# Performance work log

Hardware: AMD Instinct MI355X
Metric: run time of the kernel (lower is better)

The kernel has to match this reference:

```python
import jax, jax.numpy as jnp
import numpy as np

B = 1024            # batch of CIFAR images (== number of routed tokens, seq_len is 1)
D = 768             # d_model (switch-base-8)
FF = 3072           # d_ff
E = 8               # num experts
L = 12              # encoder layers; odd-indexed layers are sparse MoE (sparse_step=2)
NM = L // 2         # 6 MoE layers and 6 dense FFN layers
NUM_CLASSES = 10


def setup_inputs() -> dict:
    key = jax.random.key(0)
    ks = jax.random.split(key, 12)
    s = 0.02
    return {
        "x": jax.random.normal(ks[0], (B, 3, 32, 32), jnp.float32),
        "proj_w": jax.random.normal(ks[1], (3 * 32 * 32, D), jnp.float32) * s,
        "proj_b": jnp.zeros((D,), jnp.float32),
        "ln1_w": jnp.ones((L, D), jnp.float32),
        "wv": jax.random.normal(ks[2], (L, D, D), jnp.float32) * s,
        "wo": jax.random.normal(ks[3], (L, D, D), jnp.float32) * s,
        "ln2_w": jnp.ones((L, D), jnp.float32),
        "dwi": jax.random.normal(ks[4], (NM, D, FF), jnp.float32) * s,
        "dwo": jax.random.normal(ks[5], (NM, FF, D), jnp.float32) * s,
        "router_w": jax.random.normal(ks[6], (NM, D, E), jnp.float32) * s,
        "ewi": jax.random.normal(ks[7], (NM, E, D, FF), jnp.float32) * s,
        "ewo": jax.random.normal(ks[8], (NM, E, FF, D), jnp.float32) * s,
        "final_ln_w": jnp.ones((D,), jnp.float32),
        "fc_w": jax.random.normal(ks[9], (D, NUM_CLASSES), jnp.float32) * s,
        "fc_b": jnp.zeros((NUM_CLASSES,), jnp.float32),
    }


def rms_norm(h, w, eps=1e-6):
    # T5LayerNorm: RMS norm, no mean subtraction, no bias
    var = jnp.mean(jnp.square(h), axis=-1, keepdims=True)
    return w * (h * jax.lax.rsqrt(var + eps))


def reference(x, proj_w, proj_b, ln1_w, wv, wo, ln2_w, dwi, dwo,
              router_w, ewi, ewo, final_ln_w, fc_w, fc_b):
    # flatten image, project to d_model; unsqueeze(1) in torch -> one token per image,
    # so we keep tokens as [B, D] throughout.
    h = x.reshape(x.shape[0], -1) @ proj_w + proj_b              # [B, D]
    d_i = 0
    m_i = 0
    for layer in range(L):
        # --- self-attention block. seq_len == 1 => softmax over a single key is
        #     identically 1 (for any scores / position bias), so the attention
        #     output is exactly Wo(Wv(x_norm)); q/k projections drop out of the
        #     math (and carry zero gradient).
        n = rms_norm(h, ln1_w[layer])
        h = h + (n @ wv[layer]) @ wo[layer]
        # --- feed-forward block (pre-norm, residual) ---
        n = rms_norm(h, ln2_w[layer])
        if layer % 2 == 1:
            # Switch top-1 MoE. With seq_len==1, token_priority==1 <= expert
            # capacity, so no tokens are ever dropped; every token goes to its
            # argmax expert and is scaled by the router probability.
            logits = n @ router_w[m_i]                           # [B, E]
            probs = jax.nn.softmax(logits, axis=-1)
            top_prob = jnp.max(probs, axis=-1, keepdims=True)    # [B, 1]
            disp = jax.nn.one_hot(jnp.argmax(probs, axis=-1), E, dtype=n.dtype)  # [B, E]
            # dense reference for the sparse dispatch: run every expert, then
            # combine with the one-hot routing mask (same math as gather/scatter)
            hid = jax.nn.relu(jnp.einsum('bd,edf->ebf', n, ewi[m_i]))   # [E, B, FF]
            eout = jnp.einsum('ebf,efd->ebd', hid, ewo[m_i])            # [E, B, D]
            moe = jnp.einsum('ebd,be->bd', eout, disp)                  # [B, D]
            h = h + top_prob * moe
            m_i += 1
        else:
            h = h + jax.nn.relu(n @ dwi[d_i]) @ dwo[d_i]
            d_i += 1
    h = rms_norm(h, final_ln_w)
    return h @ fc_w + fc_b                                      # [B, 10] logits
```

## Files before the change

kernel.cpp:

```cpp
#include <hip/hip_runtime.h>
#include <type_traits>

#define DEV __device__ __forceinline__

typedef _Float16 f16;
typedef __attribute__((ext_vector_type(8))) _Float16 f16x8;
typedef __attribute__((ext_vector_type(4))) float f32x4;

constexpr int NP = 48;

DEV int imin(int a, int b) { return a < b ? a : b; }

DEV int swz(int row, int colByte) { return (row * 128 + colByte) ^ ((row & 7) << 4); }

DEV void split2(float x, float y, unsigned& hi, unsigned& lo) {
  f16 hx = (f16)x, hy = (f16)y;
  f16 lx = (f16)(x - (float)hx), ly = (f16)(y - (float)hy);
  hi = (unsigned)__builtin_bit_cast(unsigned short, hx) |
       ((unsigned)__builtin_bit_cast(unsigned short, hy) << 16);
  lo = (unsigned)__builtin_bit_cast(unsigned short, lx) |
       ((unsigned)__builtin_bit_cast(unsigned short, ly) << 16);
}

DEV void lgkm_barrier() {
  asm volatile("s_waitcnt lgkmcnt(0)" ::: "memory");
  __builtin_amdgcn_s_barrier();
  asm volatile("" ::: "memory");
}

struct GArgs {
  const void* A; const void* Alo;
  const void* B; const void* Blo;
  const float* Hin; float* Hout;
  f16* O16; f16* O16lo;
  const float* rspIn; float* rspOut;
  const float* lnw;
  const float* prob; const float* bias;
  const int* perm; const int* off;
  int M, K, lda, ldb, ldo;
  long sAz, sBz, sOz;
  long zA, zB, zH;
  int KS;
};

template<int TM,int TN,int WR,int WC,int AM,int BMD,int CM,bool RESID,bool BIAS,bool EXPERT>
DEV void gk_body(GArgs a) {
  constexpr int TK = 64;
  constexpr int NT = 256;
  static_assert(WR * WC == 4, "4 waves per block");
  constexpr int WTM = TM / WR, WTN = TN / WC;
  constexpr int FM = WTM / 16, FN = WTN / 16;
  constexpr bool APAIR = (AM == 0);
  constexpr int UA = APAIR ? (TM * (TK / 8)) / NT : (TM * (TK / 4)) / NT;
  constexpr int UB = (TN * (TK / 4)) / NT;

  __shared__ __align__(16) f16 As[2 * TM * TK];
  __shared__ __align__(16) f16 Bs[2 * TN * TK];
  __shared__ __align__(16) f16 AsL[2 * TM * TK];
  __shared__ __align__(16) f16 BsL[2 * TN * TK];
  __shared__ float rrlds[(AM == 2 || AM == 3) ? TM : 1];

  const int tid = threadIdx.x;
  const int lane = tid & 63;
  const int wid = tid >> 6;
  const int wr = wid / WC, wc = wid % WC;

  int m0;
  int sEnd = 0x7fffffff;
  const char* Ab = (const char*)a.A;
  const char* AbL = (const char*)a.Alo;
  const char* Bb = (const char*)a.B;
  f16* O = a.O16;
  f16* OL = a.O16lo;
  float* HoutP = a.Hout;
  {
    int z = blockIdx.z;
    int e = z / a.KS;
    int kc = z - e * a.KS;
    if constexpr (EXPERT) {
      int o0 = a.off[e], o1 = a.off[e + 1];
      if ((int)blockIdx.y * TM >= o1 - o0) return;
      m0 = o0 + blockIdx.y * TM;
      sEnd = o1;
      Bb += (long)e * a.sBz * 4 + (long)kc * a.zB;
      Ab += (long)kc * a.zA;
      AbL += (long)kc * a.zA;
    } else {
      m0 = blockIdx.y * TM;
      Ab += (long)e * a.sAz * 4 + (long)kc * a.zA;
      AbL += (long)kc * a.zA;
      Bb += (long)e * a.sBz * 4 + (long)kc * a.zB;
    }
    if constexpr (CM == 4) HoutP += (long)kc * a.zH;
  }
  const int n0 = blockIdx.x * TN;

  if constexpr (AM == 2 || AM == 3) {
    if (tid < TM) {
      int s = m0 + tid;
      int row = (AM == 3) ? a.perm[imin(s, a.M - 1)] : imin(s, a.M - 1);
      float ss = 0.f;
      #pragma unroll
      for (int j = 0; j < NP; ++j) ss += a.rspIn[row * NP + j];
      rrlds[tid] = rsqrtf(ss * (1.f / 768.f) + 1e-6f);
    }
  }

  int arow[UA];
  #pragma unroll
  for (int u = 0; u < UA; ++u) {
    int id = tid + u * NT;
    if constexpr (AM == 0) arow[u] = imin(m0 + (id >> 3), a.M - 1);
    else if constexpr (AM == 3) arow[u] = a.perm[imin(m0 + (id >> 4), a.M - 1)];
    else arow[u] = imin(m0 + (id >> 4), a.M - 1);
  }

  using ARt = typename std::conditional<APAIR, int4, float4>::type;
  using BRt = float4;

  auto issueA = [&](ARt* rg, ARt* rl, int k0) {
    #pragma unroll
    for (int u = 0; u < UA; ++u) {
      int id = tid + u * NT;
      if constexpr (APAIR) {
        int kq = id & 7;
        long off = ((long)arow[u] * a.lda + k0 + kq * 8) * 2;
        rg[u] = *(const int4*)(Ab + off);
        rl[u] = *(const int4*)(AbL + off);
      } else {
        int kq = id & 15;
        rg[u] = *(const float4*)(Ab + ((long)arow[u] * a.lda + k0 + kq * 4) * 4);
      }
    }
  };
  auto commitA = [&](ARt* rg, ARt* rl, int k0, int bi) {
    char* base = (char*)As + bi * (TM * 128);
    char* baseL = (char*)AsL + bi * (TM * 128);
    #pragma unroll
    for (int u = 0; u < UA; ++u) {
      int id = tid + u * NT;
      if constexpr (APAIR) {
        int m = id >> 3, kq = id & 7;
        *(int4*)(base + swz(m, kq * 16)) = rg[u];
        *(int4*)(baseL + swz(m, kq * 16)) = rl[u];
      } else {
        int m = id >> 4, kq = id & 15;
        float4 v = *(float4*)&rg[u];
        if constexpr (AM == 2 || AM == 3) {
          float rr = rrlds[m];
          const float* w = a.lnw + k0 + kq * 4;
          v.x *= rr * w[0]; v.y *= rr * w[1]; v.z *= rr * w[2]; v.w *= rr * w[3];
        }
        uint2 ph, pl;
        split2(v.x, v.y, ph.x, pl.x);
        split2(v.z, v.w, ph.y, pl.y);
        *(uint2*)(base + swz(m, kq * 8)) = ph;
        *(uint2*)(baseL + swz(m, kq * 8)) = pl;
      }
    }
  };
  auto issueB = [&](BRt* rg, int k0) {
    #pragma unroll
    for (int u = 0; u < UB; ++u) {
      int id = tid + u * NT;
      int n = id % TN, kq = id / TN;
      const float* g = (const float*)Bb;
      #pragma unroll
      for (int i = 0; i < 4; ++i)
        ((float*)&rg[u])[i] = g[(long)(k0 + kq * 4 + i) * a.ldb + (n0 + n)];
    }
  };
  auto commitB = [&](BRt* rg, int bi) {
    char* base = (char*)Bs + bi * (TN * 128);
    char* baseL = (char*)BsL + bi * (TN * 128);
    #pragma unroll
    for (int u = 0; u < UB; ++u) {
      int id = tid + u * NT;
      int n = id % TN, kq = id / TN;
      float4 v = *(float4*)&rg[u];
      uint2 ph, pl;
      split2(v.x, v.y, ph.x, pl.x);
      split2(v.z, v.w, ph.y, pl.y);
      *(uint2*)(base + swz(n, kq * 8)) = ph;
      *(uint2*)(baseL + swz(n, kq * 8)) = pl;
    }
  };

  f32x4 acc[FM][FN] = {};
  auto compute = [&](int bi) {
    const char* pA = (const char*)As + bi * (TM * 128);
    const char* pAL = (const char*)AsL + bi * (TM * 128);
    const char* pB = (const char*)Bs + bi * (TN * 128);
    const char* pBL = (const char*)BsL + bi * (TN * 128);
    #pragma unroll
    for (int kk = 0; kk < 2; ++kk) {
      const int col2 = (kk * 32 + (lane >> 4) * 8) * 2;
      f16x8 ah[FM], al[FM], bh[FN], bl[FN];
      #pragma unroll
      for (int i = 0; i < FM; ++i) {
        ah[i] = *(const f16x8*)(pA + swz(wr * WTM + i * 16 + (lane & 15), col2));
        al[i] = *(const f16x8*)(pAL + swz(wr * WTM + i * 16 + (lane & 15), col2));
      }
      #pragma unroll
      for (int j = 0; j < FN; ++j) {
        bh[j] = *(const f16x8*)(pB + swz(wc * WTN + j * 16 + (lane & 15), col2));
        bl[j] = *(const f16x8*)(pBL + swz(wc * WTN + j * 16 + (lane & 15), col2));
      }
      #pragma unroll
      for (int i = 0; i < FM; ++i)
        #pragma unroll
        for (int j = 0; j < FN; ++j) {
          f32x4 t = acc[i][j];
          t = __builtin_amdgcn_mfma_f32_16x16x32_f16(al[i], bh[j], t, 0, 0, 0);
          t = __builtin_amdgcn_mfma_f32_16x16x32_f16(ah[i], bl[j], t, 0, 0, 0);
          t = __builtin_amdgcn_mfma_f32_16x16x32_f16(ah[i], bh[j], t, 0, 0, 0);
          acc[i][j] = t;
        }
    }
  };

  ARt ag0[UA], ag1[UA], ag2[UA], al0[UA], al1[UA], al2[UA];
  BRt bg0[UB], bg1[UB], bg2[UB];
  const int ns = a.K / TK;
  issueA(ag0, al0, 0); issueB(bg0, 0);
  if (TK < a.K) { issueA(ag1, al1, TK); issueB(bg1, TK); }
  __syncthreads();
  for (int s = 0; s < ns; s += 6) {
    int k;
    { commitA(ag0, al0, (s + 0) * TK, 0); commitB(bg0, 0);
      k = (s + 2) * TK; if (k < a.K) { issueA(ag2, al2, k); issueB(bg2, k); }
      lgkm_barrier(); compute(0); }
    if (s + 1 < ns) {
      commitA(ag1, al1, (s + 1) * TK, 1); commitB(bg1, 1);
      k = (s + 3) * TK; if (k < a.K) { issueA(ag0, al0, k); issueB(bg0, k); }
      lgkm_barrier(); compute(1); }
    if (s + 2 < ns) {
      commitA(ag2, al2, (s + 2) * TK, 0); commitB(bg2, 0);
      k = (s + 4) * TK; if (k < a.K) { issueA(ag1, al1, k); issueB(bg1, k); }
      lgkm_barrier(); compute(0); }
    if (s + 3 < ns) {
      commitA(ag0, al0, (s + 3) * TK, 1); commitB(bg0, 1);
      k = (s + 5) * TK; if (k < a.K) { issueA(ag2, al2, k); issueB(bg2, k); }
      lgkm_barrier(); compute(1); }
    if (s + 4 < ns) {
      commitA(ag1, al1, (s + 4) * TK, 0); commitB(bg1, 0);
      k = (s + 6) * TK; if (k < a.K) { issueA(ag0, al0, k); issueB(bg0, k); }
      lgkm_barrier(); compute(0); }
    if (s + 5 < ns) {
      commitA(ag2, al2, (s + 5) * TK, 1); commitB(bg2, 1);
      k = (s + 7) * TK; if (k < a.K) { issueA(ag1, al1, k); issueB(bg1, k); }
      lgkm_barrier(); compute(1); }
  }

  const int cr = (lane >> 4) * 4;
  const int cc = lane & 15;
  if constexpr (CM == 0 || CM == 2) {
    #pragma unroll
    for (int i = 0; i < FM; ++i) {
      #pragma unroll
      for (int r = 0; r < 4; ++r) {
        int gm = m0 + wr * WTM + i * 16 + cr + r;
        if (gm >= sEnd) continue;
        #pragma unroll
        for (int j = 0; j < FN; ++j) {
          int gn = n0 + wc * WTN + j * 16 + cc;
          float v = acc[i][j][r];
          if constexpr (CM == 2) v = fmaxf(v, 0.f);
          f16 hv = (f16)v;
          O[(long)gm * a.ldo + gn] = hv;
          OL[(long)gm * a.ldo + gn] = (f16)(v - (float)hv);
        }
      }
    }
  } else if constexpr (CM == 4) {
    #pragma unroll
    for (int i = 0; i < FM; ++i) {
      #pragma unroll
      for (int r = 0; r < 4; ++r) {
        int s = m0 + wr * WTM + i * 16 + cr + r;
        if (s >= sEnd || s >= a.M) continue;
        #pragma unroll
        for (int j = 0; j < FN; ++j) {
          int gn = n0 + wc * WTN + j * 16 + cc;
          HoutP[(long)s * a.ldo + gn] = acc[i][j][r];
        }
      }
    }
  } else {
    #pragma unroll
    for (int i = 0; i < FM; ++i) {
      #pragma unroll
      for (int r = 0; r < 4; ++r) {
        int s = m0 + wr * WTM + i * 16 + cr + r;
        int grow = s;
        float p = 1.f;
        bool ok = true;
        if constexpr (CM == 3) {
          ok = s < sEnd;
          int t = a.perm[imin(s, a.M - 1)];
          grow = t;
          p = a.prob[t];
        }
        #pragma unroll
        for (int j = 0; j < FN; ++j) {
          int gn = n0 + wc * WTN + j * 16 + cc;
          float v = acc[i][j][r];
          if constexpr (CM == 3) v *= p;
          if constexpr (BIAS) v += a.bias[gn];
          if constexpr (RESID) v += a.Hin[(long)grow * 768 + gn];
          if constexpr (CM == 3) v += a.Hin[(long)grow * 768 + gn];
          if (ok) a.Hout[(long)grow * 768 + gn] = v;
          float ssum = v * v;
          ssum += __shfl_xor(ssum, 1); ssum += __shfl_xor(ssum, 2);
          ssum += __shfl_xor(ssum, 4); ssum += __shfl_xor(ssum, 8);
          if (ok && (lane & 15) == 0)
            a.rspOut[(long)grow * NP + ((n0 + wc * WTN + j * 16) >> 4)] = ssum;
        }
      }
    }
  }
}

__global__ __launch_bounds__(256, 3) void k_wct(GArgs a)  { gk_body<32,64,2,2, 1,1,4, false,false,false>(a); }
__global__ __launch_bounds__(256, 3) void k_proj(GArgs a) { gk_body<32,64,2,2, 1,1,1, false,true, false>(a); }
__global__ __launch_bounds__(256, 3) void k_attn(GArgs a) { gk_body<32,32,2,2, 2,1,1, true, false,false>(a); }
__global__ __launch_bounds__(256, 3) void k_ffn1(GArgs a) { gk_body<32,64,2,2, 2,1,2, false,false,false>(a); }
__global__ __launch_bounds__(256, 3) void k_ffn2(GArgs a) { gk_body<32,64,2,2, 0,1,1, true, false,false>(a); }
__global__ __launch_bounds__(256, 3) void k_eg1(GArgs a)  { gk_body<64,32,2,2, 3,1,2, false,false,true>(a); }
__global__ __launch_bounds__(256, 3) void k_eg2(GArgs a)  { gk_body<32,64,2,2, 0,1,3, false,false,true>(a); }

__global__ __launch_bounds__(256)
void rs_k(const float* H, const float* rsp, const float* lnw, const float* rw,
          int* eid, float* prob, int* off, int* perm, int* done) {
  int tid = threadIdx.x;
  int lane = tid & 63;
  int row = blockIdx.x * 4 + (tid >> 6);
  float ss = 0.f;
  #pragma unroll
  for (int j = 0; j < NP; ++j) ss += rsp[row * NP + j];
  float rr = rsqrtf(ss * (1.f / 768.f) + 1e-6f);
  float le[8] = {0, 0, 0, 0, 0, 0, 0, 0};
  #pragma unroll
  for (int i = 0; i < 12; ++i) {
    int k = i * 64 + lane;
    float n = H[row * 768 + k] * rr * lnw[k];
    const float* w = rw + k * 8;
    float4 w0 = *(const float4*)w, w1 = *(const float4*)(w + 4);
    le[0] += n * w0.x; le[1] += n * w0.y; le[2] += n * w0.z; le[3] += n * w0.w;
    le[4] += n * w1.x; le[5] += n * w1.y; le[6] += n * w1.z; le[7] += n * w1.w;
  }
  #pragma unroll
  for (int m = 1; m < 64; m <<= 1) {
    #pragma unroll
    for (int e = 0; e < 8; ++e) le[e] += __shfl_xor(le[e], m);
  }
  if (lane == 0) {
    float mx = le[0]; int am = 0;
    #pragma unroll
    for (int e = 1; e < 8; ++e) if (le[e] > mx) { mx = le[e]; am = e; }
    float den = 0.f;
    #pragma unroll
    for (int e = 0; e < 8; ++e) den += expf(le[e] - mx);
    eid[row] = am; prob[row] = 1.f / den;
  }
  __threadfence();
  __shared__ int ticket;
  if (tid == 0) ticket = atomicAdd(done, 1);
  __syncthreads();
  if (ticket != (int)gridDim.x - 1) return;
  __threadfence();
  __shared__ int cnt[8], c2[8], offs[9];
  if (tid < 8) { cnt[tid] = 0; c2[tid] = 0; }
  __syncthreads();
  for (int t = tid; t < 1024; t += 256) atomicAdd(&cnt[eid[t]], 1);
  __syncthreads();
  if (tid == 0) {
    int acc = 0;
    for (int e = 0; e < 8; ++e) { offs[e] = acc; off[e] = acc; acc += cnt[e]; }
    offs[8] = acc; off[8] = acc;
    *done = 0;
  }
  __syncthreads();
  for (int t = tid; t < 1024; t += 256) {
    int e = eid[t];
    int r = atomicAdd(&c2[e], 1);
    perm[offs[e] + r] = t;
  }
}

__global__ __launch_bounds__(256)
void fc_k(const float* H, const float* rsp, const float* lnw, const float* fw,
          const float* fb, float* out) {
  int lane = threadIdx.x & 63;
  int row = blockIdx.x * 4 + (threadIdx.x >> 6);
  float ss = 0.f;
  #pragma unroll
  for (int j = 0; j < NP; ++j) ss += rsp[row * NP + j];
  float rr = rsqrtf(ss * (1.f / 768.f) + 1e-6f);
  float acc[10] = {0, 0, 0, 0, 0, 0, 0, 0, 0, 0};
  #pragma unroll
  for (int i = 0; i < 12; ++i) {
    int k = i * 64 + lane;
    float n = H[row * 768 + k] * rr * lnw[k];
    const float* w = fw + k * 10;
    #pragma unroll
    for (int c = 0; c < 10; ++c) acc[c] += n * w[c];
  }
  #pragma unroll
  for (int m = 1; m < 64; m <<= 1) {
    #pragma unroll
    for (int c = 0; c < 10; ++c) acc[c] += __shfl_xor(acc[c], m);
  }
  if (lane == 0) {
    #pragma unroll
    for (int c = 0; c < 10; ++c) out[row * 10 + c] = acc[c] + fb[c];
  }
}

extern "C" void kernel_launch(void* const* d_in, const int* in_sizes, int n_in,
                              void* d_out, int out_size, void* d_ws, size_t ws_size,
                              hipStream_t stream) {
  const float* x     = (const float*)d_in[0];
  const float* projw = (const float*)d_in[1];
  const float* projb = (const float*)d_in[2];
  const float* ln1   = (const float*)d_in[3];
  const float* wvp   = (const float*)d_in[4];
  const float* wop   = (const float*)d_in[5];
  const float* ln2   = (const float*)d_in[6];
  const float* dwi   = (const float*)d_in[7];
  const float* dwo   = (const float*)d_in[8];
  const float* rw    = (const float*)d_in[9];
  const float* ewi   = (const float*)d_in[10];
  const float* ewo   = (const float*)d_in[11];
  const float* flnw  = (const float*)d_in[12];
  const float* fcw   = (const float*)d_in[13];
  const float* fcb   = (const float*)d_in[14];

  char* ws = (char*)d_ws;
  float* hA   = (float*)(ws);
  float* hB   = (float*)(ws + 3145728);
  f16*   hidH = (f16*)(ws + 6291456);
  f16*   hidL = (f16*)(ws + 12582912);
  float* rsp  = (float*)(ws + 18874368);
  int*   eid  = (int*)(ws + 23789568);
  float* prob = (float*)(ws + 23793664);
  int*   perm = (int*)(ws + 23797760);
  int*   off  = (int*)(ws + 23801856);
  int*   done = (int*)(ws + 23802112);
  float* wct  = (float*)(ws + 36385280);
  if (ws_size < 36385280u) return;
  const bool useWct = ws_size >= 64696832u;
  auto slot = [&](int s) { return rsp + (long)s * 1024 * NP; };

  hipMemsetAsync(done, 0, 4, stream);

  if (useWct) {
    GArgs g{}; g.A = wvp; g.B = wop; g.Hout = wct; g.KS = 12;
    g.M = 768; g.K = 768; g.lda = 768; g.ldb = 768; g.ldo = 768;
    g.zA = (long)589824 * 4; g.zB = (long)589824 * 4; g.zH = 589824;
    k_wct<<<dim3(12,24,12), 256, 0, stream>>>(g);
  }
  {
    GArgs g{}; g.A = x; g.B = projw; g.Hout = hA; g.bias = projb; g.rspOut = slot(0); g.KS = 1;
    g.M = 1024; g.K = 3072; g.lda = 3072; g.ldb = 768; g.ldo = 768;
    k_proj<<<dim3(12,32,1), 256, 0, stream>>>(g);
  }
  for (int l = 0; l < 12; ++l) {
    if (useWct) {
      GArgs g{}; g.A = hA; g.B = wct + (long)l * 589824;
      g.Hin = hA; g.Hout = hB; g.KS = 1;
      g.rspIn = slot(2*l); g.rspOut = slot(2*l+1); g.lnw = ln1 + l * 768;
      g.M = 1024; g.K = 768; g.lda = 768; g.ldb = 768;
      k_attn<<<dim3(24,32,1), 256, 0, stream>>>(g);
    } else {
      {
        GArgs g{}; g.A = hA; g.B = wvp + (long)l * 589824;
        g.O16 = hidH; g.O16lo = hidL; g.KS = 1;
        g.rspIn = slot(2*l); g.lnw = ln1 + l * 768;
        g.M = 1024; g.K = 768; g.lda = 768; g.ldb = 768; g.ldo = 768;
        k_ffn1<<<dim3(12,32,1), 256, 0, stream>>>(g);
      }
      {
        GArgs g{}; g.A = hidH; g.Alo = hidL; g.B = wop + (long)l * 589824;
        g.Hin = hA; g.Hout = hB; g.rspOut = slot(2*l+1); g.KS = 1;
        g.M = 1024; g.K = 768; g.lda = 768; g.ldb = 768;
        k_ffn2<<<dim3(12,32,1), 256, 0, stream>>>(g);
      }
    }
    if ((l & 1) == 0) {
      int di = l / 2;
      {
        GArgs g{}; g.A = hB; g.B = dwi + (long)di * 768 * 3072;
        g.O16 = hidH; g.O16lo = hidL; g.KS = 1;
        g.rspIn = slot(2*l+1); g.lnw = ln2 + l * 768;
        g.M = 1024; g.K = 768; g.lda = 768; g.ldb = 3072; g.ldo = 3072;
        k_ffn1<<<dim3(48,32,1), 256, 0, stream>>>(g);
      }
      {
        GArgs g{}; g.A = hidH; g.Alo = hidL; g.B = dwo + (long)di * 3072 * 768;
        g.Hin = hB; g.Hout = hA; g.rspOut = slot(2*l+2); g.KS = 1;
        g.M = 1024; g.K = 3072; g.lda = 3072; g.ldb = 768;
        k_ffn2<<<dim3(12,32,1), 256, 0, stream>>>(g);
      }
    } else {
      int mi = l / 2;
      rs_k<<<dim3(256), 256, 0, stream>>>(hB, slot(2*l+1), ln2 + l * 768,
                                          rw + (long)mi * 768 * 8, eid, prob, off, perm, done);
      {
        GArgs g{}; g.A = hB; g.B = ewi + (long)mi * 8 * 768 * 3072;
        g.O16 = hidH; g.O16lo = hidL; g.perm = perm; g.off = off; g.KS = 1;
        g.rspIn = slot(2*l+1); g.lnw = ln2 + l * 768;
        g.M = 1024; g.K = 768; g.lda = 768; g.ldb = 3072; g.ldo = 3072;
        g.sBz = (long)768 * 3072;
        k_eg1<<<dim3(96,16,8), 256, 0, stream>>>(g);
      }
      {
        GArgs g{}; g.A = hidH; g.Alo = hidL; g.B = ewo + (long)mi * 8 * 3072 * 768;
        g.Hin = hB; g.Hout = hA; g.rspOut = slot(2*l+2);
        g.perm = perm; g.prob = prob; g.off = off; g.KS = 1;
        g.M = 1024; g.K = 3072; g.lda = 3072; g.ldb = 768;
        g.sBz = (long)3072 * 768;
        k_eg2<<<dim3(12,32,8), 256, 0, stream>>>(g);
      }
    }
  }
  fc_k<<<dim3(256), 256, 0, stream>>>(hA, slot(24), flnw, fcw, fcb, (float*)d_out);
}
```

Measured before the change: 2.006 ms.

## Split-K the K=3072 down-projection GEMMs with fused last-block reduction

The projection, dense FFN down-projection and expert down-projection GEMMs (K=3072) are split into 4 K-chunks that write partial sums to a slab buffer. For proj and dense FFN, the last block of each row band, found with an atomic counter, sums the partials and applies bias, residual and the RMS partial-sum epilogue. For experts, a separate reduction kernel applies the router-prob scaling, the scatter through perm and the residual. The goal is more parallelism and higher occupancy on the 12x32 grids, at the cost of extra slab traffic, atomics and an extra launch; the fallback non-Wct path now also reuses k_attn.

```diff
diff --git a/kernel.cpp b/kernel.cpp
--- a/kernel.cpp
+++ b/kernel.cpp
@@ -32,11 +32,13 @@
   const void* A; const void* Alo;
   const void* B; const void* Blo;
   const float* Hin; float* Hout;
+  float* Hfin;
   f16* O16; f16* O16lo;
   const float* rspIn; float* rspOut;
   const float* lnw;
   const float* prob; const float* bias;
   const int* perm; const int* off;
+  int* cnt; int nWr;
   int M, K, lda, ldb, ldo;
   long sAz, sBz, sOz;
   long zA, zB, zH;
@@ -91,7 +93,7 @@
       AbL += (long)kc * a.zA;
       Bb += (long)e * a.sBz * 4 + (long)kc * a.zB;
     }
-    if constexpr (CM == 4) HoutP += (long)kc * a.zH;
+    if constexpr (CM == 4 || CM == 5) HoutP += (long)kc * a.zH;
   }
   const int n0 = blockIdx.x * TN;
 
@@ -272,7 +274,7 @@
         }
       }
     }
-  } else if constexpr (CM == 4) {
+  } else if constexpr (CM == 4 || CM == 5) {
     #pragma unroll
     for (int i = 0; i < FM; ++i) {
       #pragma unroll
@@ -283,6 +285,44 @@
         for (int j = 0; j < FN; ++j) {
           int gn = n0 + wc * WTN + j * 16 + cc;
           HoutP[(long)s * a.ldo + gn] = acc[i][j][r];
+        }
+      }
+    }
+    if constexpr (CM == 5) {
+      __threadfence();
+      __shared__ int tick;
+      if (tid == 0) tick = atomicAdd(a.cnt + blockIdx.y, 1);
+      __syncthreads();
+      if (tick == a.nWr - 1) {
+        __threadfence();
+        if (tid == 0) a.cnt[blockIdx.y] = 0;
+        const float* sb = a.Hout;
+        #pragma unroll
+        for (int r = 0; r < TM / (WR * WC); ++r) {
+          int row = blockIdx.y * TM + wid * (TM / (WR * WC)) + r;
+          #pragma unroll
+          for (int p3 = 0; p3 < 3; ++p3) {
+            int c = p3 * 256 + lane * 4;
+            long o = (long)row * 768 + c;
+            float4 v  = *(const float4*)(sb + o);
+            float4 v1 = *(const float4*)(sb + a.zH + o);
+            float4 v2 = *(const float4*)(sb + 2 * a.zH + o);
+            float4 v3 = *(const float4*)(sb + 3 * a.zH + o);
+            v.x = (v.x + v1.x) + (v2.x + v3.x); v.y = (v.y + v1.y) + (v2.y + v3.y);
+            v.z = (v.z + v1.z) + (v2.z + v3.z); v.w = (v.w + v1.w) + (v2.w + v3.w);
+            if constexpr (BIAS) {
+              const float4 b = *(const float4*)(a.bias + c);
+              v.x += b.x; v.y += b.y; v.z += b.z; v.w += b.w;
+            }
+            if constexpr (RESID) {
+              const float4 h = *(const float4*)(a.Hin + o);
+              v.x += h.x; v.y += h.y; v.z += h.z; v.w += h.w;
+            }
+            *(float4*)(a.Hfin + o) = v;
+            float ss = v.x * v.x + v.y * v.y + v.z * v.z + v.w * v.w;
+            ss += __shfl_xor(ss, 1); ss += __shfl_xor(ss, 2);
+            if ((lane & 3) == 0) a.rspOut[(long)row * NP + p3 * 16 + (lane >> 2)] = ss;
+          }
         }
       }
     }
@@ -322,12 +362,44 @@
 }
 
 __global__ __launch_bounds__(256, 3) void k_wct(GArgs a)  { gk_body<32,64,2,2, 1,1,4, false,false,false>(a); }
-__global__ __launch_bounds__(256, 3) void k_proj(GArgs a) { gk_body<32,64,2,2, 1,1,1, false,true, false>(a); }
+__global__ __launch_bounds__(256, 3) void k_proj(GArgs a) { gk_body<32,64,2,2, 1,1,5, false,true, false>(a); }
 __global__ __launch_bounds__(256, 3) void k_attn(GArgs a) { gk_body<32,32,2,2, 2,1,1, true, false,false>(a); }
 __global__ __launch_bounds__(256, 3) void k_ffn1(GArgs a) { gk_body<32,64,2,2, 2,1,2, false,false,false>(a); }
-__global__ __launch_bounds__(256, 3) void k_ffn2(GArgs a) { gk_body<32,64,2,2, 0,1,1, true, false,false>(a); }
+__global__ __launch_bounds__(256, 3) void k_ffn2(GArgs a) { gk_body<32,64,2,2, 0,1,5, true, false,false>(a); }
 __global__ __launch_bounds__(256, 3) void k_eg1(GArgs a)  { gk_body<64,32,2,2, 3,1,2, false,false,true>(a); }
-__global__ __launch_bounds__(256, 3) void k_eg2(GArgs a)  { gk_body<32,64,2,2, 0,1,3, false,false,true>(a); }
+__global__ __launch_bounds__(256, 3) void k_eg2(GArgs a)  { gk_body<32,64,2,2, 0,1,4, false,false,true>(a); }
+
+__global__ __launch_bounds__(256)
+void red_k(const float* slab, long sst, const int* perm, const float* prob,
+           const float* Hin, const float* bias, float* Hout, float* rsp) {
+  int lane = threadIdx.x & 63;
+  int s = blockIdx.x * 4 + (threadIdx.x >> 6);
+  int row = perm ? perm[s] : s;
+  float p = prob ? prob[row] : 1.f;
+  #pragma unroll
+  for (int p3 = 0; p3 < 3; ++p3) {
+    int c = p3 * 256 + lane * 4;
+    float4 v = *(const float4*)(slab + (long)s * 768 + c);
+    float4 v1 = *(const float4*)(slab + sst + (long)s * 768 + c);
+    float4 v2 = *(const float4*)(slab + 2 * sst + (long)s * 768 + c);
+    float4 v3 = *(const float4*)(slab + 3 * sst + (long)s * 768 + c);
+    v.x = (v.x + v1.x) + (v2.x + v3.x); v.y = (v.y + v1.y) + (v2.y + v3.y);
+    v.z = (v.z + v1.z) + (v2.z + v3.z); v.w = (v.w + v1.w) + (v2.w + v3.w);
+    v.x *= p; v.y *= p; v.z *= p; v.w *= p;
+    if (bias) {
+      const float4 b = *(const float4*)(bias + c);
+      v.x += b.x; v.y += b.y; v.z += b.z; v.w += b.w;
+    }
+    if (Hin) {
+      const float4 h = *(const float4*)(Hin + (long)row * 768 + c);
+      v.x += h.x; v.y += h.y; v.z += h.z; v.w += h.w;
+    }
+    *(float4*)(Hout + (long)row * 768 + c) = v;
+    float ss = v.x * v.x + v.y * v.y + v.z * v.z + v.w * v.w;
+    ss += __shfl_xor(ss, 1); ss += __shfl_xor(ss, 2);
+    if ((lane & 3) == 0) rsp[(long)row * NP + p3 * 16 + (lane >> 2)] = ss;
+  }
+}
 
 __global__ __launch_bounds__(256)
 void rs_k(const float* H, const float* rsp, const float* lnw, const float* rw,
@@ -446,13 +518,17 @@
   float* prob = (float*)(ws + 23793664);
   int*   perm = (int*)(ws + 23797760);
   int*   off  = (int*)(ws + 23801856);
-  int*   done = (int*)(ws + 23802112);
+  int*   sync = (int*)(ws + 23802112);
+  float* slab = (float*)(ws + 23802368);
   float* wct  = (float*)(ws + 36385280);
   if (ws_size < 36385280u) return;
   const bool useWct = ws_size >= 64696832u;
   auto slot = [&](int s) { return rsp + (long)s * 1024 * NP; };
-
-  hipMemsetAsync(done, 0, 4, stream);
+  const long SST = 1024 * 768;
+  int* done = sync;
+  int* bandc = sync + 8;
+
+  hipMemsetAsync(sync, 0, 256, stream);
 
   if (useWct) {
     GArgs g{}; g.A = wvp; g.B = wop; g.Hout = wct; g.KS = 12;
@@ -461,9 +537,11 @@
     k_wct<<<dim3(12,24,12), 256, 0, stream>>>(g);
   }
   {
-    GArgs g{}; g.A = x; g.B = projw; g.Hout = hA; g.bias = projb; g.rspOut = slot(0); g.KS = 1;
-    g.M = 1024; g.K = 3072; g.lda = 3072; g.ldb = 768; g.ldo = 768;
-    k_proj<<<dim3(12,32,1), 256, 0, stream>>>(g);
+    GArgs g{}; g.A = x; g.B = projw; g.Hout = slab; g.Hfin = hA; g.bias = projb;
+    g.rspOut = slot(0); g.cnt = bandc; g.nWr = 48; g.KS = 4;
+    g.M = 1024; g.K = 768; g.lda = 3072; g.ldb = 768; g.ldo = 768;
+    g.zA = 768 * 4; g.zB = (long)768 * 768 * 4; g.zH = SST;
+    k_proj<<<dim3(12,32,4), 256, 0, stream>>>(g);
   }
   for (int l = 0; l < 12; ++l) {
     if (useWct) {
@@ -475,16 +553,12 @@
     } else {
       {
         GArgs g{}; g.A = hA; g.B = wvp + (long)l * 589824;
-        g.O16 = hidH; g.O16lo = hidL; g.KS = 1;
-        g.rspIn = slot(2*l); g.lnw = ln1 + l * 768;
-        g.M = 1024; g.K = 768; g.lda = 768; g.ldb = 768; g.ldo = 768;
-        k_ffn1<<<dim3(12,32,1), 256, 0, stream>>>(g);
+        g.Hin = hA; g.Hout = hB; g.KS = 1;
+        g.rspIn = slot(2*l); g.rspOut = slot(2*l+1); g.lnw = ln1 + l * 768;
+        g.M = 1024; g.K = 768; g.lda = 768; g.ldb = 768;
+        k_attn<<<dim3(24,32,1), 256, 0, stream>>>(g);
       }
       {
-        GArgs g{}; g.A = hidH; g.Alo = hidL; g.B = wop + (long)l * 589824;
-        g.Hin = hA; g.Hout = hB; g.rspOut = slot(2*l+1); g.KS = 1;
-        g.M = 1024; g.K = 768; g.lda = 768; g.ldb = 768;
-        k_ffn2<<<dim3(12,32,1), 256, 0, stream>>>(g);
       }
     }
     if ((l & 1) == 0) {
@@ -498,9 +572,11 @@
       }
       {
         GArgs g{}; g.A = hidH; g.Alo = hidL; g.B = dwo + (long)di * 3072 * 768;
-        g.Hin = hB; g.Hout = hA; g.rspOut = slot(2*l+2); g.KS = 1;
-        g.M = 1024; g.K = 3072; g.lda = 3072; g.ldb = 768;
-        k_ffn2<<<dim3(12,32,1), 256, 0, stream>>>(g);
+        g.Hout = slab; g.Hfin = hA; g.Hin = hB;
+        g.rspOut = slot(2*l+2); g.cnt = bandc; g.nWr = 48; g.KS = 4;
+        g.M = 1024; g.K = 768; g.lda = 3072; g.ldb = 768; g.ldo = 768;
+        g.zA = 768 * 2; g.zB = (long)768 * 768 * 4; g.zH = SST;
+        k_ffn2<<<dim3(12,32,4), 256, 0, stream>>>(g);
       }
     } else {
       int mi = l / 2;
@@ -516,11 +592,11 @@
       }
       {
         GArgs g{}; g.A = hidH; g.Alo = hidL; g.B = ewo + (long)mi * 8 * 3072 * 768;
-        g.Hin = hB; g.Hout = hA; g.rspOut = slot(2*l+2);
-        g.perm = perm; g.prob = prob; g.off = off; g.KS = 1;
-        g.M = 1024; g.K = 3072; g.lda = 3072; g.ldb = 768;
-        g.sBz = (long)3072 * 768;
-        k_eg2<<<dim3(12,32,8), 256, 0, stream>>>(g);
+        g.Hout = slab; g.off = off; g.KS = 4;
+        g.M = 1024; g.K = 768; g.lda = 3072; g.ldb = 768; g.ldo = 768;
+        g.sBz = (long)3072 * 768; g.zA = 768 * 2; g.zB = (long)768 * 768 * 4; g.zH = SST;
+        k_eg2<<<dim3(12,32,32), 256, 0, stream>>>(g);
+        red_k<<<dim3(256), 256, 0, stream>>>(slab, SST, perm, prob, hB, nullptr, hA, slot(2*l+2));
       }
     }
   }
```

Result: slower. 3.255 ms (+62.3%).
